# Kernel tuning notes

Hardware: AMD Instinct MI355X
Metric: run time of the kernel (lower is better)

Reference implementation:

```python
import math
import jax, jax.numpy as jnp
import numpy as np

B, T, D = 2, 1024, 512
H, DK = 8, 64


def setup_inputs() -> dict:
    key = jax.random.key(0)
    ks = jax.random.split(key, 7)
    s = 1.0 / math.sqrt(D)
    x = jax.random.normal(ks[0], (B, T, D), dtype=jnp.float32)
    Wq = jax.random.normal(ks[1], (D, H * DK), dtype=jnp.float32) * s
    Wk = jax.random.normal(ks[2], (D, H * DK), dtype=jnp.float32) * s
    Wv = jax.random.normal(ks[3], (D, H * DK), dtype=jnp.float32) * s
    Wo = jax.random.normal(ks[4], (H * DK, D), dtype=jnp.float32) * s
    Wg = jax.random.normal(ks[5], (D, H * DK), dtype=jnp.float32) * 0.02
    bg = jnp.ones((H * DK,), dtype=jnp.float32)  # gate_bias_init = 1.0
    return {"x": x, "Wq": Wq, "Wk": Wk, "Wv": Wv, "Wo": Wo, "Wg": Wg, "bg": bg}


def reference(x, Wq, Wk, Wv, Wo, Wg, bg):
    b, t, d = x.shape
    Q = jax.nn.relu(x @ Wq).reshape(b, t, H, DK)
    K = jax.nn.relu(x @ Wk).reshape(b, t, H, DK)
    V = (x @ Wv).reshape(b, t, H, DK)
    angle = jnp.arange(t, dtype=x.dtype) * (math.pi / (2 * t))  # (T,)
    cosw = jnp.cos(angle)[None, :, None, None]
    sinw = jnp.sin(angle)[None, :, None, None]
    Qc, Qs = Q * cosw, Q * sinw
    Kc, Ks = K * cosw, K * sinw
    # cumulative KV outer products: (B,T,H,DK,DK)
    Sc = jnp.cumsum(jnp.einsum('bthd,bthe->bthde', Kc, V), axis=1)
    Ss = jnp.cumsum(jnp.einsum('bthd,bthe->bthde', Ks, V), axis=1)
    o = jnp.einsum('bthd,bthde->bthe', Qc, Sc) + jnp.einsum('bthd,bthde->bthe', Qs, Ss)
    zc = jnp.cumsum(Kc, axis=1)
    zs = jnp.cumsum(Ks, axis=1)
    z = jnp.einsum('bthd,bthd->bth', Qc, zc) + jnp.einsum('bthd,bthd->bth', Qs, zs)
    z = jnp.maximum(z, 1e-6)[..., None]
    o = o / z
    gate = jax.nn.sigmoid((x @ Wg + bg).reshape(b, t, H, DK))
    o = o * gate
    return o.reshape(b, t, H * DK) @ Wo
```

## Files before the change

### kernel.cpp

```cpp
#include <hip/hip_runtime.h>
#include <math.h>

#define B_ 2
#define T_ 1024
#define D_ 512
#define H_ 8
#define DK_ 64
#define NBH_ 16
#define C_ 32
#define G_ 32

#define PI_OVER_2T 0.00153398078788564122971808758949f

typedef float f32x4 __attribute__((ext_vector_type(4)));
typedef short s16x8 __attribute__((ext_vector_type(8)));

__device__ __forceinline__ ushort f2bf(float x) {
    unsigned u = __float_as_uint(x);
    unsigned r = (u + 0x7fffu + ((u >> 16) & 1u)) >> 16;
    return (ushort)r;
}
__device__ __forceinline__ float bf2f(ushort u) {
    return __uint_as_float((unsigned)u << 16);
}

__device__ __forceinline__ void async16(void* lds, const void* g) {
    __builtin_amdgcn_global_load_lds(
        (const __attribute__((address_space(1))) void*)g,
        (__attribute__((address_space(3))) void*)lds, 16, 0, 0);
}

__global__ __launch_bounds__(256) void k_conv(
    const float* __restrict__ x,
    const float* __restrict__ Wq, const float* __restrict__ Wk,
    const float* __restrict__ Wv, const float* __restrict__ Wg,
    const float* __restrict__ Wo,
    ushort* __restrict__ xb, ushort* __restrict__ WtAll)
{
    __shared__ float Ts[64][65];
    const int bx = blockIdx.x;
    const int tid = threadIdx.x;
    if (bx < 1024) {
        int i = (bx * 256 + tid) * 4;
        float4 v = *(const float4*)&x[i];
        ushort4 o;
        o.x = f2bf(v.x); o.y = f2bf(v.y); o.z = f2bf(v.z); o.w = f2bf(v.w);
        *(ushort4*)&xb[i] = o;
        return;
    }
    const int bid = bx - 1024;
    const int mi = bid >> 6;
    const int t64 = bid & 63;
    const float* __restrict__ W = (mi == 0) ? Wq : (mi == 1) ? Wk
                                 : (mi == 2) ? Wv : (mi == 3) ? Wg : Wo;
    const int tr = t64 >> 3, tc = t64 & 7;
#pragma unroll
    for (int p = 0; p < 4; p++) {
        int row = p * 16 + (tid >> 4);
        int c4 = (tid & 15) * 4;
        float4 v = *(const float4*)&W[(size_t)(tr * 64 + row) * 512 + tc * 64 + c4];
        Ts[row][c4 + 0] = v.x; Ts[row][c4 + 1] = v.y;
        Ts[row][c4 + 2] = v.z; Ts[row][c4 + 3] = v.w;
    }
    __syncthreads();
    const int nl = tid >> 2, kc = (tid & 3) * 16;
    ushort buf[16];
#pragma unroll
    for (int u = 0; u < 16; u++) buf[u] = f2bf(Ts[kc + u][nl]);
    ushort* dst = WtAll + (size_t)mi * 262144 + (size_t)(tc * 64 + nl) * 512
                  + tr * 64 + kc;
    *(uint4*)dst = *(uint4*)&buf[0];
    *(uint4*)(dst + 8) = *(uint4*)&buf[8];
}

__global__ __launch_bounds__(256) void k_g0(
    const ushort* __restrict__ A, const ushort* __restrict__ WtAll,
    const float* __restrict__ bg,
    ushort* __restrict__ Qg, ushort* __restrict__ Kg,
    ushort* __restrict__ Vg, ushort* __restrict__ Gg,
    ushort* __restrict__ Sst, float* __restrict__ Zst)
{
    __shared__ union {
        struct { ushort As[2][64 * 64]; ushort Bs[2][2 * 64 * 64]; } s;
        struct { ushort KcT[64 * 72]; ushort KsT[64 * 72];
                 ushort VT[64 * 72]; ushort KR[64 * 72];
                 ushort VR[64 * 72]; } e;
    } sm;
    __shared__ float cosR[64], sinR[64];

    const int tid = threadIdx.x;
    const int ct = blockIdx.x;
    const int rowBase = blockIdx.y * 64;
    const bool isKV = (ct >= 8);
    const int matCol = (ct & 7) * 64;
    const ushort* __restrict__ B0 = WtAll + (size_t)(isKV ? 1 : 0) * 262144;
    const ushort* __restrict__ B1 = WtAll + (size_t)(isKV ? 2 : 3) * 262144;

    const int wave = tid >> 6, lane = tid & 63;
    const int q = lane >> 4, ln = lane & 15;
    const int mB = (wave >> 1) * 32, nB = (wave & 1) * 32;

    int fu[2];
    const ushort* gA[2];
    const ushort* gB0[2];
    const ushort* gB1[2];
#pragma unroll
    for (int u = 0; u < 2; u++) {
        int f = tid * 8 + u * 2048;
        int r = f >> 6;
        int gc = ((f >> 3) & 7) ^ (r & 7);
        fu[u] = f;
        gA[u]  = A  + (size_t)(rowBase + r) * 512 + gc * 8;
        gB0[u] = B0 + (size_t)(matCol + r) * 512 + gc * 8;
        gB1[u] = B1 + (size_t)(matCol + r) * 512 + gc * 8;
    }

    f32x4 accA[2][2], accB[2][2];
#pragma unroll
    for (int i = 0; i < 2; i++)
#pragma unroll
        for (int j = 0; j < 2; j++) {
            accA[i][j] = (f32x4){0.f, 0.f, 0.f, 0.f};
            accB[i][j] = (f32x4){0.f, 0.f, 0.f, 0.f};
        }

    int aoff[2][2], boff[2][2];
#pragma unroll
    for (int i = 0; i < 2; i++) {
        int ra = mB + i * 16 + ln;
#pragma unroll
        for (int ks = 0; ks < 2; ks++)
            aoff[i][ks] = ra * 64 + (((ks * 4 + q) ^ (ra & 7)) * 8);
    }
#pragma unroll
    for (int j = 0; j < 2; j++) {
        int rb = nB + j * 16 + ln;
#pragma unroll
        for (int ks = 0; ks < 2; ks++)
            boff[j][ks] = rb * 64 + (((ks * 4 + q) ^ (rb & 7)) * 8);
    }

#pragma unroll
    for (int u = 0; u < 2; u++) {
        async16(&sm.s.As[0][fu[u]], gA[u]);
        async16(&sm.s.Bs[0][fu[u]], gB0[u]);
        async16(&sm.s.Bs[0][4096 + fu[u]], gB1[u]);
    }

    int cur = 0;
    for (int kb = 0; kb < 512; kb += 64) {
        __syncthreads();
        if (kb + 64 < 512) {
            int nxt = cur ^ 1;
#pragma unroll
            for (int u = 0; u < 2; u++) {
                async16(&sm.s.As[nxt][fu[u]], gA[u] + kb + 64);
                async16(&sm.s.Bs[nxt][fu[u]], gB0[u] + kb + 64);
                async16(&sm.s.Bs[nxt][4096 + fu[u]], gB1[u] + kb + 64);
            }
        }
#pragma unroll
        for (int ks = 0; ks < 2; ks++) {
            s16x8 af[2], b0f[2], b1f[2];
#pragma unroll
            for (int i = 0; i < 2; i++)
                af[i] = *(const s16x8*)&sm.s.As[cur][aoff[i][ks]];
#pragma unroll
            for (int j = 0; j < 2; j++) {
                b0f[j] = *(const s16x8*)&sm.s.Bs[cur][boff[j][ks]];
                b1f[j] = *(const s16x8*)&sm.s.Bs[cur][4096 + boff[j][ks]];
            }
#pragma unroll
            for (int i = 0; i < 2; i++)
#pragma unroll
                for (int j = 0; j < 2; j++) {
                    accA[i][j] = __builtin_amdgcn_mfma_f32_16x16x32_bf16(
                        af[i], b0f[j], accA[i][j], 0, 0, 0);
                    accB[i][j] = __builtin_amdgcn_mfma_f32_16x16x32_bf16(
                        af[i], b1f[j], accB[i][j], 0, 0, 0);
                }
        }
        cur ^= 1;
    }
    if (isKV && tid < 64) {
        float a = (float)((rowBase + tid) & 1023) * PI_OVER_2T;
        cosR[tid] = cosf(a);
        sinR[tid] = sinf(a);
    }
    __syncthreads();

    if (!isKV) {
        ushort* QT = sm.e.KcT;
        ushort* GT = sm.e.KsT;
#pragma unroll
        for (int i = 0; i < 2; i++)
#pragma unroll
            for (int j = 0; j < 2; j++) {
                int colL = nB + j * 16 + ln;
                float bgv = bg[matCol + colL];
#pragma unroll
                for (int r = 0; r < 4; r++) {
                    int rowL = mB + i * 16 + q * 4 + r;
                    QT[rowL * 72 + colL] = f2bf(fmaxf(accA[i][j][r], 0.f));
                    GT[rowL * 72 + colL] =
                        f2bf(1.f / (1.f + expf(-(accB[i][j][r] + bgv))));
                }
            }
        __syncthreads();
#pragma unroll
        for (int it = 0; it < 2; it++) {
            int row = it * 32 + (tid >> 3), sub = tid & 7;
            uint4 qv = *(const uint4*)&QT[row * 72 + sub * 8];
            uint4 gv = *(const uint4*)&GT[row * 72 + sub * 8];
            size_t go = (size_t)(rowBase + row) * 512 + matCol + sub * 8;
            *(uint4*)&Qg[go] = qv;
            *(uint4*)&Gg[go] = gv;
        }
        return;
    }

    const int h = ct - 8;
    const int b = rowBase >> 10;
    const int c = wave >> 1;
    const int gG = ((rowBase & 1023) >> 5) + c;
    const int blk = (b * 8 + h) * 32 + gG;

    float zc[2] = {0.f, 0.f}, zs[2] = {0.f, 0.f};
#pragma unroll
    for (int i = 0; i < 2; i++)
#pragma unroll
        for (int r = 0; r < 4; r++) {
            int tLoc = mB + i * 16 + q * 4 + r;
            float ca = cosR[tLoc], sa = sinR[tLoc];
#pragma unroll
            for (int j = 0; j < 2; j++) {
                int col = nB + j * 16 + ln;
                float kv = fmaxf(accA[i][j][r], 0.f);
                float vv = accB[i][j][r];
                sm.e.KR[tLoc * 72 + col] = f2bf(kv);
                sm.e.VR[tLoc * 72 + col] = f2bf(vv);
                float kc = kv * ca, ks = kv * sa;
                sm.e.KcT[col * 72 + tLoc] = f2bf(kc);
                sm.e.KsT[col * 72 + tLoc] = f2bf(ks);
                sm.e.VT [col * 72 + tLoc] = f2bf(vv);
                zc[j] += kc; zs[j] += ks;
            }
        }
#pragma unroll
    for (int j = 0; j < 2; j++) {
        zc[j] += __shfl_xor(zc[j], 16); zc[j] += __shfl_xor(zc[j], 32);
        zs[j] += __shfl_xor(zs[j], 16); zs[j] += __shfl_xor(zs[j], 32);
    }
    if (q == 0) {
#pragma unroll
        for (int j = 0; j < 2; j++) {
            int d = nB + j * 16 + ln;
            Zst[(size_t)blk * 128 + d] = zc[j];
            Zst[(size_t)blk * 128 + 64 + d] = zs[j];
        }
    }
    __syncthreads();

#pragma unroll
    for (int it = 0; it < 2; it++) {
        int row = it * 32 + (tid >> 3), sub = tid & 7;
        uint4 kv4 = *(const uint4*)&sm.e.KR[row * 72 + sub * 8];
        uint4 vv4 = *(const uint4*)&sm.e.VR[row * 72 + sub * 8];
        size_t go = (size_t)(rowBase + row) * 512 + h * 64 + sub * 8;
        *(uint4*)&Kg[go] = kv4;
        *(uint4*)&Vg[go] = vv4;
    }

    {
        const int eh = (wave & 1) * 32;
        ushort* Sp = Sst + (size_t)blk * 8192;
        s16x8 av[2];
#pragma unroll
        for (int fi = 0; fi < 2; fi++)
            av[fi] = *(const s16x8*)&sm.e.VT[(eh + fi * 16 + ln) * 72
                                            + c * 32 + q * 8];
#pragma unroll
        for (int fj = 0; fj < 4; fj++) {
            s16x8 bc = *(const s16x8*)&sm.e.KcT[(fj * 16 + ln) * 72
                                                + c * 32 + q * 8];
            s16x8 bs = *(const s16x8*)&sm.e.KsT[(fj * 16 + ln) * 72
                                                + c * 32 + q * 8];
#pragma unroll
            for (int fi = 0; fi < 2; fi++) {
                f32x4 sc = __builtin_amdgcn_mfma_f32_16x16x32_bf16(
                    av[fi], bc, (f32x4){0.f, 0.f, 0.f, 0.f}, 0, 0, 0);
                f32x4 ss = __builtin_amdgcn_mfma_f32_16x16x32_bf16(
                    av[fi], bs, (f32x4){0.f, 0.f, 0.f, 0.f}, 0, 0, 0);
#pragma unroll
                for (int rr = 0; rr < 4; rr++) {
                    int e = eh + fi * 16 + q * 4 + rr;
                    int d = fj * 16 + ln;
                    Sp[e * 64 + d] = f2bf(sc[rr]);
                    Sp[4096 + e * 64 + d] = f2bf(ss[rr]);
                }
            }
        }
    }
}

template<int MODE, int TM, int TN, int BK>
__global__ __launch_bounds__(256) void k_gemm(
    const ushort* __restrict__ A, const ushort* __restrict__ Bt,
    const float* __restrict__ bg,
    void* __restrict__ O0v, void* __restrict__ O1v,
    void* __restrict__ O2v, void* __restrict__ O3v)
{
    constexpr int WM = TM / 2, WN = TN / 2;
    constexpr int FM = WM / 16, FN = WN / 16;
    constexpr int CH = BK / 8;
    constexpr int SH = (BK == 32) ? 1 : 0;
    constexpr int KS = BK / 32;
    constexpr int NA = TM * BK / 2048;
    constexpr int NB = TN * BK / 2048;
    static_assert(TM == 64 && TN == 32, "epilogue specialized");

    __shared__ ushort As[2][TM * BK];
    __shared__ ushort Bs[2][TN * BK];

    const int tid = threadIdx.x;
    const int ct = blockIdx.x;
    const int rowBase = blockIdx.y * TM;

    const int matCol = ct * TN;
    const ushort* __restrict__ Bmat = Bt;

    const int wave = tid >> 6, lane = tid & 63;
    const int q = lane >> 4, ln = lane & 15;
    const int mB = (wave >> 1) * WM, nB = (wave & 1) * WN;

    int fuA[NA], fuB[NB];
    const ushort* gA[NA];
    const ushort* gB[NB];
#pragma unroll
    for (int u = 0; u < NA; u++) {
        int fu = tid * 8 + u * 2048;
        int r = fu / BK;
        int slot = (fu >> 3) & (CH - 1);
        int gc = slot ^ ((r >> SH) & (CH - 1));
        fuA[u] = fu;
        gA[u] = A + (size_t)(rowBase + r) * 512 + gc * 8;
    }
#pragma unroll
    for (int u = 0; u < NB; u++) {
        int fu = tid * 8 + u * 2048;
        int r = fu / BK;
        int slot = (fu >> 3) & (CH - 1);
        int gc = slot ^ ((r >> SH) & (CH - 1));
        fuB[u] = fu;
        gB[u] = Bmat + (size_t)(matCol + r) * 512 + gc * 8;
    }

    f32x4 acc[FM][FN];
#pragma unroll
    for (int i = 0; i < FM; i++)
#pragma unroll
        for (int j = 0; j < FN; j++) acc[i][j] = (f32x4){0.f, 0.f, 0.f, 0.f};

    int aoff[FM][KS], boff[FN][KS];
#pragma unroll
    for (int i = 0; i < FM; i++) {
        int ra = mB + i * 16 + ln;
#pragma unroll
        for (int ks = 0; ks < KS; ks++)
            aoff[i][ks] = ra * BK + (((ks * 4 + q) ^ ((ra >> SH) & (CH - 1))) * 8);
    }
#pragma unroll
    for (int j = 0; j < FN; j++) {
        int rb = nB + j * 16 + ln;
#pragma unroll
        for (int ks = 0; ks < KS; ks++)
            boff[j][ks] = rb * BK + (((ks * 4 + q) ^ ((rb >> SH) & (CH - 1))) * 8);
    }

#pragma unroll
    for (int u = 0; u < NA; u++) async16(&As[0][fuA[u]], gA[u]);
#pragma unroll
    for (int u = 0; u < NB; u++) async16(&Bs[0][fuB[u]], gB[u]);

    int cur = 0;
    for (int kb = 0; kb < 512; kb += BK) {
        __syncthreads();
        if (kb + BK < 512) {
#pragma unroll
            for (int u = 0; u < NA; u++)
                async16(&As[cur ^ 1][fuA[u]], gA[u] + kb + BK);
#pragma unroll
            for (int u = 0; u < NB; u++)
                async16(&Bs[cur ^ 1][fuB[u]], gB[u] + kb + BK);
        }
#pragma unroll
        for (int ks = 0; ks < KS; ks++) {
            s16x8 af[FM], bf[FN];
#pragma unroll
            for (int i = 0; i < FM; i++)
                af[i] = *(const s16x8*)&As[cur][aoff[i][ks]];
#pragma unroll
            for (int j = 0; j < FN; j++)
                bf[j] = *(const s16x8*)&Bs[cur][boff[j][ks]];
#pragma unroll
            for (int i = 0; i < FM; i++)
#pragma unroll
                for (int j = 0; j < FN; j++)
                    acc[i][j] = __builtin_amdgcn_mfma_f32_16x16x32_bf16(
                        af[i], bf[j], acc[i][j], 0, 0, 0);
        }
        cur ^= 1;
    }
    __syncthreads();

    float* Ot = (float*)&As[0][0];
#pragma unroll
    for (int i = 0; i < FM; i++)
#pragma unroll
        for (int j = 0; j < FN; j++) {
            int colL = nB + j * 16 + ln;
#pragma unroll
            for (int r = 0; r < 4; r++) {
                int rowL = mB + i * 16 + q * 4 + r;
                Ot[rowL * 36 + colL] = acc[i][j][r];
            }
        }
    __syncthreads();

    float* __restrict__ Out = (float*)O0v;
    {
        int row = tid >> 2, sub = tid & 3;
        float4 a0 = *(const float4*)&Ot[row * 36 + sub * 8];
        float4 a1 = *(const float4*)&Ot[row * 36 + sub * 8 + 4];
        size_t go = (size_t)(rowBase + row) * 512 + matCol + sub * 8;
        *(float4*)&Out[go] = a0;
        *(float4*)&Out[go + 4] = a1;
    }
}

__global__ __launch_bounds__(256) void k_scan(
    ushort* __restrict__ Sst, float* __restrict__ Zst)
{
    int id = blockIdx.x * 256 + threadIdx.x;
    if (id < 32768) {
        int bh = id >> 11, i4 = (id & 2047) * 4;
        size_t base = (size_t)bh * (G_ * 8192) + i4;
        ushort4 v[G_];
#pragma unroll
        for (int g = 0; g < G_; g++)
            v[g] = *(const ushort4*)&Sst[base + (size_t)g * 8192];
        float rx = 0.f, ry = 0.f, rz = 0.f, rw = 0.f;
#pragma unroll
        for (int g = 0; g < G_; g++) {
            ushort4 t = v[g];
            ushort4 o;
            o.x = f2bf(rx); o.y = f2bf(ry); o.z = f2bf(rz); o.w = f2bf(rw);
            *(ushort4*)&Sst[base + (size_t)g * 8192] = o;
            rx += bf2f(t.x); ry += bf2f(t.y);
            rz += bf2f(t.z); rw += bf2f(t.w);
        }
    } else {
        int id2 = id - 32768;
        if (id2 >= 512) return;
        int bh = id2 >> 5, i4 = (id2 & 31) * 4;
        size_t base = (size_t)bh * (G_ * 128) + i4;
        float4 v[G_];
#pragma unroll
        for (int g = 0; g < G_; g++)
            v[g] = *(const float4*)&Zst[base + (size_t)g * 128];
        float4 run = make_float4(0.f, 0.f, 0.f, 0.f);
#pragma unroll
        for (int g = 0; g < G_; g++) {
            float4 t = v[g];
            *(float4*)&Zst[base + (size_t)g * 128] = run;
            run.x += t.x; run.y += t.y; run.z += t.z; run.w += t.w;
        }
    }
}

__global__ __launch_bounds__(256) void k_out_chunk(
    const ushort* __restrict__ Qg, const ushort* __restrict__ Kg,
    const ushort* __restrict__ Vg, const ushort* __restrict__ Gg,
    const ushort* __restrict__ Sst, const float* __restrict__ Zst,
    ushort* __restrict__ Op)
{
    __shared__ ushort VT[64 * 40];
    __shared__ ushort Pb[32 * 40];
    __shared__ float zinv[32];
    __shared__ float Ot[32 * 68];

    const int blk = blockIdx.x;
    const int bh = blk >> 5, g = blk & 31;
    const int b = bh >> 3, h = bh & 7;
    const int tid = threadIdx.x;
    const int rBase = b * T_ + g * C_;
    const int colB = h * DK_;
    const int wave = tid >> 6, lane = tid & 63;
    const int q = lane >> 4, ln = lane & 15;

    {
        int row = tid >> 3, c8 = (tid & 7) * 8;
        uint4 vraw = *(const uint4*)&Vg[(size_t)(rBase + row) * D_ + colB + c8];
        const ushort* vp = (const ushort*)&vraw;
#pragma unroll
        for (int u = 0; u < 8; u++) VT[(c8 + u) * 40 + row] = vp[u];
    }

    const int mi = wave >> 1, njp = wave & 1;
    const ushort* qrow = Qg + (size_t)(rBase + mi * 16 + ln) * D_ + colB;
    s16x8 aq0 = *(const s16x8*)&qrow[q * 8];
    s16x8 aq1 = *(const s16x8*)&qrow[32 + q * 8];
    {
        const ushort* krow = Kg + (size_t)(rBase + njp * 16 + ln) * D_ + colB;
        s16x8 bk0 = *(const s16x8*)&krow[q * 8];
        s16x8 bk1 = *(const s16x8*)&krow[32 + q * 8];
        f32x4 pacc = __builtin_amdgcn_mfma_f32_16x16x32_bf16(
            aq0, bk0, (f32x4){0.f, 0.f, 0.f, 0.f}, 0, 0, 0);
        pacc = __builtin_amdgcn_mfma_f32_16x16x32_bf16(aq1, bk1, pacc, 0, 0, 0);
        int sl = njp * 16 + ln;
#pragma unroll
        for (int r = 0; r < 4; r++) {
            int tl = mi * 16 + q * 4 + r;
            float w = (sl <= tl) ? cosf((float)(tl - sl) * PI_OVER_2T) : 0.f;
            Pb[tl * 40 + sl] = f2bf(pacc[r] * w);
        }
    }
    __syncthreads();

    {
        int t = tid >> 3, sub = tid & 7;
        uint4 qraw = *(const uint4*)&Qg[(size_t)(rBase + t) * D_ + colB + sub * 8];
        const ushort* qp = (const ushort*)&qraw;
        const float* zcp = Zst + (size_t)blk * 128 + sub * 8;
        float4 zc0 = *(const float4*)&zcp[0];
        float4 zc1 = *(const float4*)&zcp[4];
        float4 zs0 = *(const float4*)&zcp[64];
        float4 zs1 = *(const float4*)&zcp[68];
        float pc = 0.f, ps = 0.f;
        float zcv[8] = {zc0.x, zc0.y, zc0.z, zc0.w, zc1.x, zc1.y, zc1.z, zc1.w};
        float zsv[8] = {zs0.x, zs0.y, zs0.z, zs0.w, zs1.x, zs1.y, zs1.z, zs1.w};
#pragma unroll
        for (int u = 0; u < 8; u++) {
            float qf = bf2f(qp[u]);
            pc += qf * zcv[u]; ps += qf * zsv[u];
        }
        float pr = 0.f;
#pragma unroll
        for (int u = 0; u < 4; u++) pr += bf2f(Pb[t * 40 + sub * 4 + u]);
#pragma unroll
        for (int m = 1; m < 8; m <<= 1) {
            pc += __shfl_xor(pc, m);
            ps += __shfl_xor(ps, m);
            pr += __shfl_xor(pr, m);
        }
        if (sub == 0) {
            float at = (float)(g * C_ + t) * PI_OVER_2T;
            float z = cosf(at) * pc + sinf(at) * ps + pr;
            zinv[t] = 1.f / fmaxf(z, 1e-6f);
        }
    }
    __syncthreads();

    {
        float cr[4], sr[4];
#pragma unroll
        for (int r = 0; r < 4; r++) {
            int tl = mi * 16 + q * 4 + r;
            float at = (float)(g * C_ + tl) * PI_OVER_2T;
            cr[r] = cosf(at); sr[r] = sinf(at);
        }
        s16x8 pf = *(const s16x8*)&Pb[(mi * 16 + ln) * 40 + q * 8];
        const ushort* Sp = Sst + (size_t)blk * 8192;
#pragma unroll
        for (int jj = 0; jj < 2; jj++) {
            int nj = 2 * (wave & 1) + jj;
            const ushort* scp = Sp + (nj * 16 + ln) * 64;
            s16x8 bc0 = *(const s16x8*)&scp[q * 8];
            s16x8 bc1 = *(const s16x8*)&scp[32 + q * 8];
            s16x8 bs0 = *(const s16x8*)&scp[4096 + q * 8];
            s16x8 bs1 = *(const s16x8*)&scp[4096 + 32 + q * 8];
            s16x8 bv  = *(const s16x8*)&VT[(nj * 16 + ln) * 40 + q * 8];
            f32x4 accP = __builtin_amdgcn_mfma_f32_16x16x32_bf16(
                pf, bv, (f32x4){0.f, 0.f, 0.f, 0.f}, 0, 0, 0);
            f32x4 accC = __builtin_amdgcn_mfma_f32_16x16x32_bf16(
                aq0, bc0, (f32x4){0.f, 0.f, 0.f, 0.f}, 0, 0, 0);
            accC = __builtin_amdgcn_mfma_f32_16x16x32_bf16(aq1, bc1, accC, 0, 0, 0);
            f32x4 accS = __builtin_amdgcn_mfma_f32_16x16x32_bf16(
                aq0, bs0, (f32x4){0.f, 0.f, 0.f, 0.f}, 0, 0, 0);
            accS = __builtin_amdgcn_mfma_f32_16x16x32_bf16(aq1, bs1, accS, 0, 0, 0);
#pragma unroll
            for (int r = 0; r < 4; r++) {
                int tl = mi * 16 + q * 4 + r;
                Ot[tl * 68 + nj * 16 + ln] =
                    (accP[r] + cr[r] * accC[r] + sr[r] * accS[r]) * zinv[tl];
            }
        }
    }
    __syncthreads();

    {
        int t = tid >> 3, sub = tid & 7;
        size_t go = (size_t)(rBase + t) * D_ + colB + sub * 8;
        uint4 graw = *(const uint4*)&Gg[go];
        const ushort* gp = (const ushort*)&graw;
        const float* op = &Ot[t * 68 + sub * 8];
        ushort buf[8];
#pragma unroll
        for (int u = 0; u < 8; u++)
            buf[u] = f2bf(op[u] * bf2f(gp[u]));
        *(uint4*)&Op[go] = *(uint4*)&buf[0];
    }
}

extern "C" void kernel_launch(void* const* d_in, const int* in_sizes, int n_in,
                              void* d_out, int out_size, void* d_ws, size_t ws_size,
                              hipStream_t stream)
{
    const float* x  = (const float*)d_in[0];
    const float* Wq = (const float*)d_in[1];
    const float* Wk = (const float*)d_in[2];
    const float* Wv = (const float*)d_in[3];
    const float* Wo = (const float*)d_in[4];
    const float* Wg = (const float*)d_in[5];
    const float* bg = (const float*)d_in[6];
    float* out = (float*)d_out;

    ushort* wsu = (ushort*)d_ws;
    ushort* xb    = wsu;
    ushort* WtAll = xb + 1048576;
    ushort* Qg    = WtAll + 1310720;
    ushort* Kg    = Qg + 1048576;
    ushort* Vg    = Kg + 1048576;
    ushort* Gg    = Vg + 1048576;
    ushort* Sst   = Gg + 1048576;
    ushort* Opb   = Sst + 4194304;
    float*  Zst   = (float*)(Opb + 1048576);

    dim3 blk(256);
    k_conv<<<dim3(1344), blk, 0, stream>>>(x, Wq, Wk, Wv, Wg, Wo, xb, WtAll);
    k_g0<<<dim3(16, 32), blk, 0, stream>>>(
        xb, WtAll, bg, Qg, Kg, Vg, Gg, Sst, Zst);
    k_scan<<<dim3(130), blk, 0, stream>>>(Sst, Zst);
    k_out_chunk<<<dim3(NBH_ * G_), blk, 0, stream>>>(
        Qg, Kg, Vg, Gg, Sst, Zst, Opb);
    k_gemm<1, 64, 32, 64><<<dim3(16, 32), blk, 0, stream>>>(
        Opb, WtAll + (size_t)4 * 262144, nullptr,
        out, nullptr, nullptr, nullptr);
}
```

Before: 104.7 us.

## Fuse chunk-state prefix scan into output kernel by recomputing prefix per block

Removes the separate scan kernel. Each output block now sums all preceding chunk states (and normaliser sums) for its head directly from global memory and stages the result in shared memory. This saves one kernel launch and the scan's read-modify-write pass. In exchange, total state reads grow quadratically with chunk count: about 16x more reads on average, with late chunks doing up to 31 sequential loads. This creates load imbalance.

```diff
diff --git a/kernel.cpp b/kernel.cpp
--- a/kernel.cpp
+++ b/kernel.cpp
@@ -303,6 +303,182 @@
     }
 }
 
+__global__ __launch_bounds__(256) void k_out_chunk(
+    const ushort* __restrict__ Qg, const ushort* __restrict__ Kg,
+    const ushort* __restrict__ Vg, const ushort* __restrict__ Gg,
+    const ushort* __restrict__ Sst, const float* __restrict__ Zst,
+    ushort* __restrict__ Op)
+{
+    __shared__ ushort VT[64 * 40];
+    __shared__ ushort Pb[32 * 40];
+    __shared__ float zinv[32];
+    __shared__ float Ot[32 * 68];
+    __shared__ float Zpre[128];
+    __shared__ ushort SpC[64 * 72];
+    __shared__ ushort SpS[64 * 72];
+
+    const int blk = blockIdx.x;
+    const int bh = blk >> 5, g = blk & 31;
+    const int b = bh >> 3, h = bh & 7;
+    const int tid = threadIdx.x;
+    const int rBase = b * T_ + g * C_;
+    const int colB = h * DK_;
+    const int wave = tid >> 6, lane = tid & 63;
+    const int q = lane >> 4, ln = lane & 15;
+
+    {
+        int row = tid >> 3, c8 = (tid & 7) * 8;
+        uint4 vraw = *(const uint4*)&Vg[(size_t)(rBase + row) * D_ + colB + c8];
+        const ushort* vp = (const ushort*)&vraw;
+#pragma unroll
+        for (int u = 0; u < 8; u++) VT[(c8 + u) * 40 + row] = vp[u];
+    }
+
+    {
+        float acc[8][4];
+#pragma unroll
+        for (int rep = 0; rep < 8; rep++)
+#pragma unroll
+            for (int c4 = 0; c4 < 4; c4++) acc[rep][c4] = 0.f;
+
+        const ushort* Sbase = Sst + (size_t)bh * (G_ * 8192);
+        for (int gp = 0; gp < g; gp++) {
+            const ushort* Sp_ = Sbase + (size_t)gp * 8192;
+#pragma unroll
+            for (int rep = 0; rep < 8; rep++) {
+                ushort4 v = *(const ushort4*)&Sp_[rep * 1024 + tid * 4];
+                acc[rep][0] += bf2f(v.x);
+                acc[rep][1] += bf2f(v.y);
+                acc[rep][2] += bf2f(v.z);
+                acc[rep][3] += bf2f(v.w);
+            }
+        }
+#pragma unroll
+        for (int rep = 0; rep < 8; rep++) {
+            int off = rep * 1024 + tid * 4;
+            int idx = off & 4095;
+            int e = idx >> 6, d = idx & 63;
+            ushort4 o;
+            o.x = f2bf(acc[rep][0]); o.y = f2bf(acc[rep][1]);
+            o.z = f2bf(acc[rep][2]); o.w = f2bf(acc[rep][3]);
+            ushort* dst = ((rep < 4) ? SpC : SpS) + e * 72 + d;
+            *(ushort4*)dst = o;
+        }
+    }
+
+    if (tid < 128) {
+        float s = 0.f;
+        const float* Zb = Zst + (size_t)bh * (G_ * 128) + tid;
+        for (int gp = 0; gp < g; gp++) s += Zb[(size_t)gp * 128];
+        Zpre[tid] = s;
+    }
+
+    const int mi = wave >> 1, njp = wave & 1;
+    const ushort* qrow = Qg + (size_t)(rBase + mi * 16 + ln) * D_ + colB;
+    s16x8 aq0 = *(const s16x8*)&qrow[q * 8];
+    s16x8 aq1 = *(const s16x8*)&qrow[32 + q * 8];
+    {
+        const ushort* krow = Kg + (size_t)(rBase + njp * 16 + ln) * D_ + colB;
+        s16x8 bk0 = *(const s16x8*)&krow[q * 8];
+        s16x8 bk1 = *(const s16x8*)&krow[32 + q * 8];
+        f32x4 pacc = __builtin_amdgcn_mfma_f32_16x16x32_bf16(
+            aq0, bk0, (f32x4){0.f, 0.f, 0.f, 0.f}, 0, 0, 0);
+        pacc = __builtin_amdgcn_mfma_f32_16x16x32_bf16(aq1, bk1, pacc, 0, 0, 0);
+        int sl = njp * 16 + ln;
+#pragma unroll
+        for (int r = 0; r < 4; r++) {
+            int tl = mi * 16 + q * 4 + r;
+            float w = (sl <= tl) ? cosf((float)(tl - sl) * PI_OVER_2T) : 0.f;
+            Pb[tl * 40 + sl] = f2bf(pacc[r] * w);
+        }
+    }
+    __syncthreads();
+
+    {
+        int t = tid >> 3, sub = tid & 7;
+        uint4 qraw = *(const uint4*)&Qg[(size_t)(rBase + t) * D_ + colB + sub * 8];
+        const ushort* qp = (const ushort*)&qraw;
+        const float* zcp = Zpre + sub * 8;
+        float4 zc0 = *(const float4*)&zcp[0];
+        float4 zc1 = *(const float4*)&zcp[4];
+        float4 zs0 = *(const float4*)&zcp[64];
+        float4 zs1 = *(const float4*)&zcp[68];
+        float pc = 0.f, ps = 0.f;
+        float zcv[8] = {zc0.x, zc0.y, zc0.z, zc0.w, zc1.x, zc1.y, zc1.z, zc1.w};
+        float zsv[8] = {zs0.x, zs0.y, zs0.z, zs0.w, zs1.x, zs1.y, zs1.z, zs1.w};
+#pragma unroll
+        for (int u = 0; u < 8; u++) {
+            float qf = bf2f(qp[u]);
+            pc += qf * zcv[u]; ps += qf * zsv[u];
+        }
+        float pr = 0.f;
+#pragma unroll
+        for (int u = 0; u < 4; u++) pr += bf2f(Pb[t * 40 + sub * 4 + u]);
+#pragma unroll
+        for (int m = 1; m < 8; m <<= 1) {
+            pc += __shfl_xor(pc, m);
+            ps += __shfl_xor(ps, m);
+            pr += __shfl_xor(pr, m);
+        }
+        if (sub == 0) {
+            float at = (float)(g * C_ + t) * PI_OVER_2T;
+            float z = cosf(at) * pc + sinf(at) * ps + pr;
+            zinv[t] = 1.f / fmaxf(z, 1e-6f);
+        }
+    }
+    __syncthreads();
+
+    {
+        float cr[4], sr[4];
+#pragma unroll
+        for (int r = 0; r < 4; r++) {
+            int tl = mi * 16 + q * 4 + r;
+            float at = (float)(g * C_ + tl) * PI_OVER_2T;
+            cr[r] = cosf(at); sr[r] = sinf(at);
+        }
+        s16x8 pf = *(const s16x8*)&Pb[(mi * 16 + ln) * 40 + q * 8];
+#pragma unroll
+        for (int jj = 0; jj < 2; jj++) {
+            int nj = 2 * (wave & 1) + jj;
+            const ushort* scp = SpC + (nj * 16 + ln) * 72;
+            const ushort* ssp = SpS + (nj * 16 + ln) * 72;
+            s16x8 bc0 = *(const s16x8*)&scp[q * 8];
+            s16x8 bc1 = *(const s16x8*)&scp[32 + q * 8];
+            s16x8 bs0 = *(const s16x8*)&ssp[q * 8];
+            s16x8 bs1 = *(const s16x8*)&ssp[32 + q * 8];
+            s16x8 bv  = *(const s16x8*)&VT[(nj * 16 + ln) * 40 + q * 8];
+            f32x4 accP = __builtin_amdgcn_mfma_f32_16x16x32_bf16(
+                pf, bv, (f32x4){0.f, 0.f, 0.f, 0.f}, 0, 0, 0);
+            f32x4 accC = __builtin_amdgcn_mfma_f32_16x16x32_bf16(
+                aq0, bc0, (f32x4){0.f, 0.f, 0.f, 0.f}, 0, 0, 0);
+            accC = __builtin_amdgcn_mfma_f32_16x16x32_bf16(aq1, bc1, accC, 0, 0, 0);
+            f32x4 accS = __builtin_amdgcn_mfma_f32_16x16x32_bf16(
+                aq0, bs0, (f32x4){0.f, 0.f, 0.f, 0.f}, 0, 0, 0);
+            accS = __builtin_amdgcn_mfma_f32_16x16x32_bf16(aq1, bs1, accS, 0, 0, 0);
+#pragma unroll
+            for (int r = 0; r < 4; r++) {
+                int tl = mi * 16 + q * 4 + r;
+                Ot[tl * 68 + nj * 16 + ln] =
+                    (accP[r] + cr[r] * accC[r] + sr[r] * accS[r]) * zinv[tl];
+            }
+        }
+    }
+    __syncthreads();
+
+    {
+        int t = tid >> 3, sub = tid & 7;
+        size_t go = (size_t)(rBase + t) * D_ + colB + sub * 8;
+        uint4 graw = *(const uint4*)&Gg[go];
+        const ushort* gp = (const ushort*)&graw;
+        const float* op = &Ot[t * 68 + sub * 8];
+        ushort buf[8];
+#pragma unroll
+        for (int u = 0; u < 8; u++)
+            buf[u] = f2bf(op[u] * bf2f(gp[u]));
+        *(uint4*)&Op[go] = *(uint4*)&buf[0];
+    }
+}
+
 template<int MODE, int TM, int TN, int BK>
 __global__ __launch_bounds__(256) void k_gemm(
     const ushort* __restrict__ A, const ushort* __restrict__ Bt,
@@ -438,180 +614,6 @@
     }
 }
 
-__global__ __launch_bounds__(256) void k_scan(
-    ushort* __restrict__ Sst, float* __restrict__ Zst)
-{
-    int id = blockIdx.x * 256 + threadIdx.x;
-    if (id < 32768) {
-        int bh = id >> 11, i4 = (id & 2047) * 4;
-        size_t base = (size_t)bh * (G_ * 8192) + i4;
-        ushort4 v[G_];
-#pragma unroll
-        for (int g = 0; g < G_; g++)
-            v[g] = *(const ushort4*)&Sst[base + (size_t)g * 8192];
-        float rx = 0.f, ry = 0.f, rz = 0.f, rw = 0.f;
-#pragma unroll
-        for (int g = 0; g < G_; g++) {
-            ushort4 t = v[g];
-            ushort4 o;
-            o.x = f2bf(rx); o.y = f2bf(ry); o.z = f2bf(rz); o.w = f2bf(rw);
-            *(ushort4*)&Sst[base + (size_t)g * 8192] = o;
-            rx += bf2f(t.x); ry += bf2f(t.y);
-            rz += bf2f(t.z); rw += bf2f(t.w);
-        }
-    } else {
-        int id2 = id - 32768;
-        if (id2 >= 512) return;
-        int bh = id2 >> 5, i4 = (id2 & 31) * 4;
-        size_t base = (size_t)bh * (G_ * 128) + i4;
-        float4 v[G_];
-#pragma unroll
-        for (int g = 0; g < G_; g++)
-            v[g] = *(const float4*)&Zst[base + (size_t)g * 128];
-        float4 run = make_float4(0.f, 0.f, 0.f, 0.f);
-#pragma unroll
-        for (int g = 0; g < G_; g++) {
-            float4 t = v[g];
-            *(float4*)&Zst[base + (size_t)g * 128] = run;
-            run.x += t.x; run.y += t.y; run.z += t.z; run.w += t.w;
-        }
-    }
-}
-
-__global__ __launch_bounds__(256) void k_out_chunk(
-    const ushort* __restrict__ Qg, const ushort* __restrict__ Kg,
-    const ushort* __restrict__ Vg, const ushort* __restrict__ Gg,
-    const ushort* __restrict__ Sst, const float* __restrict__ Zst,
-    ushort* __restrict__ Op)
-{
-    __shared__ ushort VT[64 * 40];
-    __shared__ ushort Pb[32 * 40];
-    __shared__ float zinv[32];
-    __shared__ float Ot[32 * 68];
-
-    const int blk = blockIdx.x;
-    const int bh = blk >> 5, g = blk & 31;
-    const int b = bh >> 3, h = bh & 7;
-    const int tid = threadIdx.x;
-    const int rBase = b * T_ + g * C_;
-    const int colB = h * DK_;
-    const int wave = tid >> 6, lane = tid & 63;
-    const int q = lane >> 4, ln = lane & 15;
-
-    {
-        int row = tid >> 3, c8 = (tid & 7) * 8;
-        uint4 vraw = *(const uint4*)&Vg[(size_t)(rBase + row) * D_ + colB + c8];
-        const ushort* vp = (const ushort*)&vraw;
-#pragma unroll
-        for (int u = 0; u < 8; u++) VT[(c8 + u) * 40 + row] = vp[u];
-    }
-
-    const int mi = wave >> 1, njp = wave & 1;
-    const ushort* qrow = Qg + (size_t)(rBase + mi * 16 + ln) * D_ + colB;
-    s16x8 aq0 = *(const s16x8*)&qrow[q * 8];
-    s16x8 aq1 = *(const s16x8*)&qrow[32 + q * 8];
-    {
-        const ushort* krow = Kg + (size_t)(rBase + njp * 16 + ln) * D_ + colB;
-        s16x8 bk0 = *(const s16x8*)&krow[q * 8];
-        s16x8 bk1 = *(const s16x8*)&krow[32 + q * 8];
-        f32x4 pacc = __builtin_amdgcn_mfma_f32_16x16x32_bf16(
-            aq0, bk0, (f32x4){0.f, 0.f, 0.f, 0.f}, 0, 0, 0);
-        pacc = __builtin_amdgcn_mfma_f32_16x16x32_bf16(aq1, bk1, pacc, 0, 0, 0);
-        int sl = njp * 16 + ln;
-#pragma unroll
-        for (int r = 0; r < 4; r++) {
-            int tl = mi * 16 + q * 4 + r;
-            float w = (sl <= tl) ? cosf((float)(tl - sl) * PI_OVER_2T) : 0.f;
-            Pb[tl * 40 + sl] = f2bf(pacc[r] * w);
-        }
-    }
-    __syncthreads();
-
-    {
-        int t = tid >> 3, sub = tid & 7;
-        uint4 qraw = *(const uint4*)&Qg[(size_t)(rBase + t) * D_ + colB + sub * 8];
-        const ushort* qp = (const ushort*)&qraw;
-        const float* zcp = Zst + (size_t)blk * 128 + sub * 8;
-        float4 zc0 = *(const float4*)&zcp[0];
-        float4 zc1 = *(const float4*)&zcp[4];
-        float4 zs0 = *(const float4*)&zcp[64];
-        float4 zs1 = *(const float4*)&zcp[68];
-        float pc = 0.f, ps = 0.f;
-        float zcv[8] = {zc0.x, zc0.y, zc0.z, zc0.w, zc1.x, zc1.y, zc1.z, zc1.w};
-        float zsv[8] = {zs0.x, zs0.y, zs0.z, zs0.w, zs1.x, zs1.y, zs1.z, zs1.w};
-#pragma unroll
-        for (int u = 0; u < 8; u++) {
-            float qf = bf2f(qp[u]);
-            pc += qf * zcv[u]; ps += qf * zsv[u];
-        }
-        float pr = 0.f;
-#pragma unroll
-        for (int u = 0; u < 4; u++) pr += bf2f(Pb[t * 40 + sub * 4 + u]);
-#pragma unroll
-        for (int m = 1; m < 8; m <<= 1) {
-            pc += __shfl_xor(pc, m);
-            ps += __shfl_xor(ps, m);
-            pr += __shfl_xor(pr, m);
-        }
-        if (sub == 0) {
-            float at = (float)(g * C_ + t) * PI_OVER_2T;
-            float z = cosf(at) * pc + sinf(at) * ps + pr;
-            zinv[t] = 1.f / fmaxf(z, 1e-6f);
-        }
-    }
-    __syncthreads();
-
-    {
-        float cr[4], sr[4];
-#pragma unroll
-        for (int r = 0; r < 4; r++) {
-            int tl = mi * 16 + q * 4 + r;
-            float at = (float)(g * C_ + tl) * PI_OVER_2T;
-            cr[r] = cosf(at); sr[r] = sinf(at);
-        }
-        s16x8 pf = *(const s16x8*)&Pb[(mi * 16 + ln) * 40 + q * 8];
-        const ushort* Sp = Sst + (size_t)blk * 8192;
-#pragma unroll
-        for (int jj = 0; jj < 2; jj++) {
-            int nj = 2 * (wave & 1) + jj;
-            const ushort* scp = Sp + (nj * 16 + ln) * 64;
-            s16x8 bc0 = *(const s16x8*)&scp[q * 8];
-            s16x8 bc1 = *(const s16x8*)&scp[32 + q * 8];
-            s16x8 bs0 = *(const s16x8*)&scp[4096 + q * 8];
-            s16x8 bs1 = *(const s16x8*)&scp[4096 + 32 + q * 8];
-            s16x8 bv  = *(const s16x8*)&VT[(nj * 16 + ln) * 40 + q * 8];
-            f32x4 accP = __builtin_amdgcn_mfma_f32_16x16x32_bf16(
-                pf, bv, (f32x4){0.f, 0.f, 0.f, 0.f}, 0, 0, 0);
-            f32x4 accC = __builtin_amdgcn_mfma_f32_16x16x32_bf16(
-                aq0, bc0, (f32x4){0.f, 0.f, 0.f, 0.f}, 0, 0, 0);
-            accC = __builtin_amdgcn_mfma_f32_16x16x32_bf16(aq1, bc1, accC, 0, 0, 0);
-            f32x4 accS = __builtin_amdgcn_mfma_f32_16x16x32_bf16(
-                aq0, bs0, (f32x4){0.f, 0.f, 0.f, 0.f}, 0, 0, 0);
-            accS = __builtin_amdgcn_mfma_f32_16x16x32_bf16(aq1, bs1, accS, 0, 0, 0);
-#pragma unroll
-            for (int r = 0; r < 4; r++) {
-                int tl = mi * 16 + q * 4 + r;
-                Ot[tl * 68 + nj * 16 + ln] =
-                    (accP[r] + cr[r] * accC[r] + sr[r] * accS[r]) * zinv[tl];
-            }
-        }
-    }
-    __syncthreads();
-
-    {
-        int t = tid >> 3, sub = tid & 7;
-        size_t go = (size_t)(rBase + t) * D_ + colB + sub * 8;
-        uint4 graw = *(const uint4*)&Gg[go];
-        const ushort* gp = (const ushort*)&graw;
-        const float* op = &Ot[t * 68 + sub * 8];
-        ushort buf[8];
-#pragma unroll
-        for (int u = 0; u < 8; u++)
-            buf[u] = f2bf(op[u] * bf2f(gp[u]));
-        *(uint4*)&Op[go] = *(uint4*)&buf[0];
-    }
-}
-
 extern "C" void kernel_launch(void* const* d_in, const int* in_sizes, int n_in,
                               void* d_out, int out_size, void* d_ws, size_t ws_size,
                               hipStream_t stream)
@@ -640,7 +642,6 @@
     k_conv<<<dim3(1344), blk, 0, stream>>>(x, Wq, Wk, Wv, Wg, Wo, xb, WtAll);
     k_g0<<<dim3(16, 32), blk, 0, stream>>>(
         xb, WtAll, bg, Qg, Kg, Vg, Gg, Sst, Zst);
-    k_scan<<<dim3(130), blk, 0, stream>>>(Sst, Zst);
     k_out_chunk<<<dim3(NBH_ * G_), blk, 0, stream>>>(
         Qg, Kg, Vg, Gg, Sst, Zst, Opb);
     k_gemm<1, 64, 32, 64><<<dim3(16, 32), blk, 0, stream>>>(
```

New measurement: 116.1 us. 1.11x slower.
